# Kernel optimization log

Hardware: AMD Instinct MI355X
Metric: run time of the kernel (lower is better)

The kernel has to match this reference:

```python
import jax, jax.numpy as jnp
import numpy as np

NUM_NODES = 50000
HIDDEN = 128
NUM_REL = 8
NUM_EDGES = 600000


def setup_inputs() -> dict:
    key = jax.random.key(0)
    ks = jax.random.split(key, 10)
    s = 1.0 / np.sqrt(HIDDEN)
    return {
        "edge_index": jax.random.randint(ks[0], (2, NUM_EDGES), 0, NUM_NODES, dtype=jnp.int32),
        "edge_type": jax.random.randint(ks[1], (NUM_EDGES,), 0, NUM_REL, dtype=jnp.int32),
        "node_emb": jax.random.normal(ks[2], (NUM_NODES, HIDDEN), jnp.float32),
        "W1": jax.random.normal(ks[3], (NUM_REL, HIDDEN, HIDDEN), jnp.float32) * s,
        "root1": jax.random.normal(ks[4], (HIDDEN, HIDDEN), jnp.float32) * s,
        "b1": jnp.zeros((HIDDEN,), jnp.float32),
        "W2": jax.random.normal(ks[5], (NUM_REL, HIDDEN, HIDDEN), jnp.float32) * s,
        "root2": jax.random.normal(ks[6], (HIDDEN, HIDDEN), jnp.float32) * s,
        "b2": jnp.zeros((HIDDEN,), jnp.float32),
    }


def rgcn_layer(x, W, root, bias, src, dst, rel):
    # PyG RGCNConv: per-relation MEAN aggregation of neighbor features,
    # transformed by relation weight, plus root transform and bias.
    N = x.shape[0]
    R = W.shape[0]
    # transform node features by every relation weight: [N, R, F]
    xw = jnp.einsum('nd,rdf->nrf', x, W)
    # per-(dst, relation) in-edge counts for mean normalization
    cnt = jnp.zeros((N, R), x.dtype).at[dst, rel].add(1.0)
    inv = 1.0 / jnp.maximum(cnt, 1.0)
    # per-edge message, normalized by destination's per-relation degree
    msg = xw[src, rel] * inv[dst, rel][:, None]  # [E, F]
    agg = jnp.zeros((N, W.shape[2]), x.dtype).at[dst].add(msg)
    return agg + x @ root + bias


def reference(edge_index, edge_type, node_emb, W1, root1, b1, W2, root2, b2):
    src, dst = edge_index[0], edge_index[1]
    h = jax.nn.relu(rgcn_layer(node_emb, W1, root1, b1, src, dst, edge_type))
    out = rgcn_layer(h, W2, root2, b2, src, dst, edge_type)
    return out
```

## Files before the change

kernel.cpp:

```cpp
#include <hip/hip_runtime.h>

#define H 128
#define RREL 8
#define NJ 9

typedef short bf16x8 __attribute__((ext_vector_type(8)));
typedef float f32x4 __attribute__((ext_vector_type(4)));
typedef unsigned short u16x8 __attribute__((ext_vector_type(8)));

static __device__ __forceinline__ unsigned short f2bf(float f) {
    unsigned int u = __float_as_uint(f);
    unsigned int r = (u + 0x7fffu + ((u >> 16) & 1u)) >> 16;
    return (unsigned short)r;
}
static __device__ __forceinline__ float bf2f(unsigned short u) {
    return __uint_as_float(((unsigned int)u) << 16);
}

__global__ void zero_kernel(int* p, long n) {
    long i = (long)blockIdx.x * blockDim.x + threadIdx.x;
    long stride = (long)gridDim.x * blockDim.x;
    for (; i < n; i += stride) p[i] = 0;
}

__global__ void count_kernel(const int* __restrict__ ei, const int* __restrict__ et,
                             int* __restrict__ cnt, int E) {
    int e = blockIdx.x * 256 + threadIdx.x;
    if (e >= E) return;
    int d = ei[E + e];
    int r = et[e];
    atomicAdd(&cnt[(size_t)d * RREL + r], 1);
}

__global__ void scan_block_kernel(const int* __restrict__ cnt, int* __restrict__ rploc,
                                  int* __restrict__ bsum, int N) {
    __shared__ int s[256];
    int t = threadIdx.x;
    int d = blockIdx.x * 256 + t;
    int v = 0;
    if (d < N) {
#pragma unroll
        for (int r = 0; r < RREL; ++r) v += cnt[(size_t)d * RREL + r];
    }
    s[t] = v;
    __syncthreads();
#pragma unroll
    for (int off = 1; off < 256; off <<= 1) {
        int u = 0;
        if (t >= off) u = s[t - off];
        __syncthreads();
        s[t] += u;
        __syncthreads();
    }
    if (d < N) rploc[d] = s[t] - v;
    if (t == 255) bsum[blockIdx.x] = s[255];
}

__global__ void scan_top_kernel(const int* __restrict__ bsum, int* __restrict__ boff, int nb) {
    __shared__ int s[256];
    int t = threadIdx.x;
    int v = (t < nb) ? bsum[t] : 0;
    s[t] = v;
    __syncthreads();
#pragma unroll
    for (int off = 1; off < 256; off <<= 1) {
        int u = 0;
        if (t >= off) u = s[t - off];
        __syncthreads();
        s[t] += u;
        __syncthreads();
    }
    boff[t] = s[t] - v;
}

__global__ void finalize_kernel(const int* __restrict__ cnt, const int* __restrict__ rploc,
                                const int* __restrict__ boff, int* __restrict__ rowptr,
                                float* __restrict__ inv, int N) {
    int d = blockIdx.x * 256 + threadIdx.x;
    if (d >= N) return;
    int rp = rploc[d] + boff[d >> 8];
    rowptr[d] = rp;
    int deg = 0;
#pragma unroll
    for (int r = 0; r < RREL; ++r) {
        int c = cnt[(size_t)d * RREL + r];
        inv[(size_t)d * RREL + r] = 1.0f / (float)max(c, 1);
        deg += c;
    }
    if (d == N - 1) rowptr[N] = rp + deg;
}

__global__ void fill_kernel(const int* __restrict__ ei, const int* __restrict__ et,
                            int* __restrict__ cursor, const int* __restrict__ rowptr,
                            int* __restrict__ packed, int E) {
    int e = blockIdx.x * 256 + threadIdx.x;
    if (e >= E) return;
    int d = ei[E + e];
    int pos = rowptr[d] + atomicAdd(&cursor[d], 1);
    packed[pos] = ei[e] | (et[e] << 20);
}

__global__ void tobf_kernel(const float* __restrict__ x, unsigned short* __restrict__ xb, long n) {
    long i = (long)blockIdx.x * blockDim.x + threadIdx.x;
    long stride = (long)gridDim.x * blockDim.x;
    for (; i < n; i += stride) xb[i] = f2bf(x[i]);
}

__global__ void wcat_kernel(const float* __restrict__ W1, const float* __restrict__ r1,
                            const float* __restrict__ W2, const float* __restrict__ r2,
                            const float* __restrict__ b1, const float* __restrict__ b2,
                            unsigned short* __restrict__ WTa1, unsigned short* __restrict__ WTa2,
                            float* __restrict__ biasP) {
    int id = blockIdx.x * 256 + threadIdx.x;
    const int per = NJ * H * H;
    if (id < per) {
        int j = id / (H * H);
        int fk = id - j * (H * H);
        int f = fk >> 7, k = fk & 127;
        float v = (j < RREL) ? W1[((size_t)j * H + k) * H + f] : r1[(size_t)k * H + f];
        WTa1[id] = f2bf(v);
        int ko = (k & 7) * 16 + (k >> 3);
        float v2 = (j < RREL) ? W2[((size_t)j * H + ko) * H + f] : r2[(size_t)ko * H + f];
        WTa2[id] = f2bf(v2);
    } else if (id < per + 2 * H) {
        int c = id - per;
        int cp = c & 127;
        int co = (cp & 7) * 16 + (cp >> 3);
        biasP[c] = (c < H) ? b1[co] : b2[co];
    }
}

__global__ __launch_bounds__(256) void xw_kernel(const unsigned short* __restrict__ xin,
                                                 const unsigned short* __restrict__ WTa,
                                                 unsigned short* __restrict__ Y,
                                                 int N, int j0, int j1) {
    __shared__ unsigned short Ws[128][136];
    const int t = threadIdx.x;
    const int w = t >> 6, l = t & 63;
    const int m_base = blockIdx.x * 128;
    const int colb = l & 15, quad = l >> 4;
    const f32x4 fz = {0.f, 0.f, 0.f, 0.f};

    int row0 = m_base + w * 32 + colb;
    int row1 = row0 + 16;
    const unsigned short* xr0 = xin + (size_t)(row0 < N ? row0 : N - 1) * H;
    const unsigned short* xr1 = xin + (size_t)(row1 < N ? row1 : N - 1) * H;

    for (int j = j0; j < j1; ++j) {
        __syncthreads();
#pragma unroll
        for (int p = 0; p < 8; ++p) {
            int c = p * 256 + t;
            int f = c >> 4, k8 = (c & 15) * 8;
            *(u16x8*)&Ws[f][k8] = *(const u16x8*)&WTa[((size_t)j * H + f) * H + k8];
        }
        __syncthreads();
        f32x4 acc[2][8];
#pragma unroll
        for (int mi = 0; mi < 2; ++mi)
#pragma unroll
            for (int n = 0; n < 8; ++n) acc[mi][n] = fz;
#pragma unroll
        for (int ks = 0; ks < 4; ++ks) {
            int kl = ks * 32 + quad * 8;
            bf16x8 a0 = *(const bf16x8*)&xr0[kl];
            bf16x8 a1 = *(const bf16x8*)&xr1[kl];
#pragma unroll
            for (int n = 0; n < 8; ++n) {
                bf16x8 b = *(const bf16x8*)&Ws[n * 16 + colb][kl];
                acc[0][n] = __builtin_amdgcn_mfma_f32_16x16x32_bf16(a0, b, acc[0][n], 0, 0, 0);
                acc[1][n] = __builtin_amdgcn_mfma_f32_16x16x32_bf16(a1, b, acc[1][n], 0, 0, 0);
            }
        }
        unsigned short* Yj = Y + (size_t)(j - j0) * N * H;
#pragma unroll
        for (int mi = 0; mi < 2; ++mi) {
#pragma unroll
            for (int i = 0; i < 4; ++i) {
                int row = m_base + w * 32 + mi * 16 + quad * 4 + i;
                if (row < N) {
                    u16x8 o;
#pragma unroll
                    for (int n = 0; n < 8; ++n) o[n] = f2bf(acc[mi][n][i]);
                    *(u16x8*)&Yj[(size_t)row * H + colb * 8] = o;
                }
            }
        }
    }
}

__global__ __launch_bounds__(256) void gather_kernel(const unsigned short* __restrict__ Y,
                                                     const float* __restrict__ inv,
                                                     const int* __restrict__ rowptr,
                                                     const int* __restrict__ packed,
                                                     const float* __restrict__ biasP,
                                                     float* __restrict__ accf,
                                                     float* __restrict__ outf,
                                                     unsigned short* __restrict__ outb,
                                                     int N, int relu, int j0, int j1, int final_pass) {
    const int t = threadIdx.x;
    const int l = t & 63;
    int d = blockIdx.x * 16 + (t >> 4);
    if (d >= N) return;
    const int fl = l & 15;
    const int kc = fl * 8;
    const int gbase = l & 48;
    int rp = 0;
    if (fl < 2) rp = rowptr[d + fl];
    float ivl = 0.f;
    if (fl < 8) ivl = inv[(size_t)d * RREL + fl];
    int beg = __shfl(rp, gbase);
    int end = __shfl(rp, gbase + 1);
    const int jr = (j1 < RREL) ? j1 : RREL;
    float tot[8] = {};
    for (int i = beg; i < end; i += 16) {
        int pk = (i + fl < end) ? packed[i + fl] : 0;
        int m = end - i;
        if (m > 16) m = 16;
        int e = 0;
        for (; e + 1 < m; e += 2) {
            int v0 = __shfl(pk, gbase + e);
            int v1 = __shfl(pk, gbase + e + 1);
            int s0 = v0 & 0xFFFFF, r0 = v0 >> 20;
            int s1 = v1 & 0xFFFFF, r1 = v1 >> 20;
            if (r0 >= j0 && r0 < jr) {
                float iv = __shfl(ivl, gbase + r0);
                u16x8 v = *(const u16x8*)&Y[((size_t)(r0 - j0) * N + s0) * H + kc];
#pragma unroll
                for (int j = 0; j < 8; ++j) tot[j] += iv * bf2f((unsigned short)v[j]);
            }
            if (r1 >= j0 && r1 < jr) {
                float iv = __shfl(ivl, gbase + r1);
                u16x8 v = *(const u16x8*)&Y[((size_t)(r1 - j0) * N + s1) * H + kc];
#pragma unroll
                for (int j = 0; j < 8; ++j) tot[j] += iv * bf2f((unsigned short)v[j]);
            }
        }
        if (e < m) {
            int v0 = __shfl(pk, gbase + e);
            int s0 = v0 & 0xFFFFF, r0 = v0 >> 20;
            if (r0 >= j0 && r0 < jr) {
                float iv = __shfl(ivl, gbase + r0);
                u16x8 v = *(const u16x8*)&Y[((size_t)(r0 - j0) * N + s0) * H + kc];
#pragma unroll
                for (int j = 0; j < 8; ++j) tot[j] += iv * bf2f((unsigned short)v[j]);
            }
        }
    }
    if (j1 == NJ) {
        u16x8 vr = *(const u16x8*)&Y[((size_t)(RREL - j0) * N + d) * H + kc];
#pragma unroll
        for (int j = 0; j < 8; ++j) tot[j] += bf2f((unsigned short)vr[j]);
    }
    if (j0 > 0) {
        f32x4 p0 = *(const f32x4*)&accf[(size_t)d * H + kc];
        f32x4 p1 = *(const f32x4*)&accf[(size_t)d * H + kc + 4];
#pragma unroll
        for (int j = 0; j < 4; ++j) { tot[j] += p0[j]; tot[4 + j] += p1[j]; }
    }
    if (final_pass) {
        f32x4 b0 = *(const f32x4*)&biasP[kc];
        f32x4 b1 = *(const f32x4*)&biasP[kc + 4];
#pragma unroll
        for (int j = 0; j < 4; ++j) { tot[j] += b0[j]; tot[4 + j] += b1[j]; }
        if (relu) {
#pragma unroll
            for (int j = 0; j < 8; ++j) tot[j] = fmaxf(tot[j], 0.f);
        }
        if (outf) {
#pragma unroll
            for (int j = 0; j < 8; ++j) outf[(size_t)d * H + j * 16 + fl] = tot[j];
        } else {
            u16x8 o;
#pragma unroll
            for (int j = 0; j < 8; ++j) o[j] = f2bf(tot[j]);
            *(u16x8*)&outb[(size_t)d * H + kc] = o;
        }
    } else {
        f32x4 o0, o1;
#pragma unroll
        for (int j = 0; j < 4; ++j) { o0[j] = tot[j]; o1[j] = tot[4 + j]; }
        *(f32x4*)&accf[(size_t)d * H + kc] = o0;
        *(f32x4*)&accf[(size_t)d * H + kc + 4] = o1;
    }
}

extern "C" void kernel_launch(void* const* d_in, const int* in_sizes, int n_in,
                              void* d_out, int out_size, void* d_ws, size_t ws_size,
                              hipStream_t stream) {
    const int* edge_index = (const int*)d_in[0];
    const int* edge_type  = (const int*)d_in[1];
    const float* node_emb = (const float*)d_in[2];
    const float* W1    = (const float*)d_in[3];
    const float* root1 = (const float*)d_in[4];
    const float* b1    = (const float*)d_in[5];
    const float* W2    = (const float*)d_in[6];
    const float* root2 = (const float*)d_in[7];
    const float* b2    = (const float*)d_in[8];
    float* out = (float*)d_out;

    const int E = in_sizes[1];
    const int N = in_sizes[2] / H;

    char* base = (char*)d_ws;
    size_t off = 0;
    auto take = [&](size_t bytes) { size_t o = off; off = (off + bytes + 63) & ~(size_t)63; return o; };
    int*   cnt     = (int*)  (base + take((size_t)N * RREL * 4));
    int*   cursor  = (int*)  (base + take((size_t)N * 4));
    int*   rploc   = (int*)  (base + take((size_t)N * 4));
    int*   bsum    = (int*)  (base + take(256 * 4));
    int*   boff    = (int*)  (base + take(256 * 4));
    int*   rowptr  = (int*)  (base + take(((size_t)N + 1) * 4));
    float* inv     = (float*)(base + take((size_t)N * RREL * 4));
    int*   packed  = (int*)  (base + take((size_t)E * 4));
    unsigned short* WTa1 = (unsigned short*)(base + take((size_t)NJ * H * H * 2));
    unsigned short* WTa2 = (unsigned short*)(base + take((size_t)NJ * H * H * 2));
    float* biasP   = (float*)(base + take(2 * H * 4));
    unsigned short* xb  = (unsigned short*)(base + take((size_t)N * H * 2));
    unsigned short* hb  = (unsigned short*)(base + take((size_t)N * H * 2));

    size_t fixed_off = off;
    unsigned short* Y;
    float* accf = nullptr;
    int rc;
    size_t availA = (ws_size > fixed_off) ? ws_size - fixed_off : 0;
    if (availA >= (size_t)NJ * N * H * 2) {
        Y = (unsigned short*)(base + fixed_off);
        rc = NJ;
    } else {
        accf = (float*)(base + fixed_off);
        size_t off2 = fixed_off + (((size_t)N * H * 4 + 63) & ~(size_t)63);
        Y = (unsigned short*)(base + off2);
        size_t availB = (ws_size > off2) ? ws_size - off2 : 0;
        rc = (int)(availB / ((size_t)N * H * 2));
        if (rc > RREL) rc = RREL;
        if (rc < 1) rc = 1;
    }

    const int nbScan = (N + 255) / 256;

    zero_kernel<<<512, 256, 0, stream>>>(cnt, (long)N * (RREL + 1));
    count_kernel<<<(E + 255) / 256, 256, 0, stream>>>(edge_index, edge_type, cnt, E);
    scan_block_kernel<<<nbScan, 256, 0, stream>>>(cnt, rploc, bsum, N);
    scan_top_kernel<<<1, 256, 0, stream>>>(bsum, boff, nbScan);
    finalize_kernel<<<nbScan, 256, 0, stream>>>(cnt, rploc, boff, rowptr, inv, N);
    fill_kernel<<<(E + 255) / 256, 256, 0, stream>>>(edge_index, edge_type, cursor, rowptr, packed, E);
    wcat_kernel<<<(NJ * H * H + 2 * H + 255) / 256, 256, 0, stream>>>(W1, root1, W2, root2, b1, b2,
                                                                      WTa1, WTa2, biasP);
    tobf_kernel<<<1024, 256, 0, stream>>>(node_emb, xb, (long)N * H);

    const int gx = (N + 127) / 128;
    const int gg = (N + 15) / 16;

    auto run_layer = [&](const unsigned short* xin, const unsigned short* WTa, const float* bp,
                         float* of, unsigned short* ob, int relu) {
        for (int j0 = 0; j0 < NJ; j0 += rc) {
            int j1 = (j0 + rc < NJ) ? j0 + rc : NJ;
            int fin = (j1 == NJ);
            xw_kernel<<<gx, 256, 0, stream>>>(xin, WTa, Y, N, j0, j1);
            gather_kernel<<<gg, 256, 0, stream>>>(Y, inv, rowptr, packed, bp, accf,
                                                  fin ? of : nullptr, fin ? ob : nullptr,
                                                  N, relu, j0, j1, fin);
        }
    };

    run_layer(xb, WTa1, biasP, nullptr, hb, 1);
    run_layer(hb, WTa2, biasP + H, out, nullptr, 0);
}
```

Before: 282.1 us.

## Aggregate-then-transform: fuse per-relation gather and GEMM into one layer kernel

Reorders the RGCN computation so raw neighbor features are first summed per (destination, relation) in shared memory, then multiplied by the concatenated relation and root weights with MFMA. This removes the per-relation transformed tensor Y (nine N×H bf16 arrays) and its write and read traffic, and leaves one kernel launch per layer. Edges are now sorted by relation within each destination, using per-(node, relation) row pointers and cursors, so the run-length accumulation works. The cost is a large shared-memory tile per block, which limits occupancy, weights are read from global memory without reuse in LDS, and the per-relation mean is rounded to bf16 before the GEMM.

```diff
diff --git a/kernel.cpp b/kernel.cpp
--- a/kernel.cpp
+++ b/kernel.cpp
@@ -3,6 +3,8 @@
 #define H 128
 #define RREL 8
 #define NJ 9
+#define MT 32
+#define LROW 1160
 
 typedef short bf16x8 __attribute__((ext_vector_type(8)));
 typedef float f32x4 __attribute__((ext_vector_type(4)));
@@ -75,29 +77,32 @@
 
 __global__ void finalize_kernel(const int* __restrict__ cnt, const int* __restrict__ rploc,
                                 const int* __restrict__ boff, int* __restrict__ rowptr,
-                                float* __restrict__ inv, int N) {
+                                int* __restrict__ rowptr2, float* __restrict__ inv, int N) {
     int d = blockIdx.x * 256 + threadIdx.x;
     if (d >= N) return;
     int rp = rploc[d] + boff[d >> 8];
     rowptr[d] = rp;
-    int deg = 0;
+    int run = rp;
 #pragma unroll
     for (int r = 0; r < RREL; ++r) {
         int c = cnt[(size_t)d * RREL + r];
+        rowptr2[(size_t)d * RREL + r] = run;
         inv[(size_t)d * RREL + r] = 1.0f / (float)max(c, 1);
-        deg += c;
-    }
-    if (d == N - 1) rowptr[N] = rp + deg;
+        run += c;
+    }
+    if (d == N - 1) rowptr[N] = run;
 }
 
 __global__ void fill_kernel(const int* __restrict__ ei, const int* __restrict__ et,
-                            int* __restrict__ cursor, const int* __restrict__ rowptr,
+                            int* __restrict__ cursor, const int* __restrict__ rowptr2,
                             int* __restrict__ packed, int E) {
     int e = blockIdx.x * 256 + threadIdx.x;
     if (e >= E) return;
     int d = ei[E + e];
-    int pos = rowptr[d] + atomicAdd(&cursor[d], 1);
-    packed[pos] = ei[e] | (et[e] << 20);
+    int r = et[e];
+    size_t bin = (size_t)d * RREL + r;
+    int pos = rowptr2[bin] + atomicAdd(&cursor[bin], 1);
+    packed[pos] = ei[e] | (r << 20);
 }
 
 __global__ void tobf_kernel(const float* __restrict__ x, unsigned short* __restrict__ xb, long n) {
@@ -117,171 +122,139 @@
         int j = id / (H * H);
         int fk = id - j * (H * H);
         int f = fk >> 7, k = fk & 127;
-        float v = (j < RREL) ? W1[((size_t)j * H + k) * H + f] : r1[(size_t)k * H + f];
-        WTa1[id] = f2bf(v);
-        int ko = (k & 7) * 16 + (k >> 3);
-        float v2 = (j < RREL) ? W2[((size_t)j * H + ko) * H + f] : r2[(size_t)ko * H + f];
+        float v1 = (j < RREL) ? W1[((size_t)j * H + k) * H + f] : r1[(size_t)k * H + f];
+        WTa1[id] = f2bf(v1);
+        float v2 = (j < RREL) ? W2[((size_t)j * H + k) * H + f] : r2[(size_t)k * H + f];
         WTa2[id] = f2bf(v2);
     } else if (id < per + 2 * H) {
         int c = id - per;
-        int cp = c & 127;
-        int co = (cp & 7) * 16 + (cp >> 3);
-        biasP[c] = (c < H) ? b1[co] : b2[co];
-    }
-}
-
-__global__ __launch_bounds__(256) void xw_kernel(const unsigned short* __restrict__ xin,
-                                                 const unsigned short* __restrict__ WTa,
-                                                 unsigned short* __restrict__ Y,
-                                                 int N, int j0, int j1) {
-    __shared__ unsigned short Ws[128][136];
-    const int t = threadIdx.x;
-    const int w = t >> 6, l = t & 63;
-    const int m_base = blockIdx.x * 128;
-    const int colb = l & 15, quad = l >> 4;
-    const f32x4 fz = {0.f, 0.f, 0.f, 0.f};
-
-    int row0 = m_base + w * 32 + colb;
-    int row1 = row0 + 16;
-    const unsigned short* xr0 = xin + (size_t)(row0 < N ? row0 : N - 1) * H;
-    const unsigned short* xr1 = xin + (size_t)(row1 < N ? row1 : N - 1) * H;
-
-    for (int j = j0; j < j1; ++j) {
-        __syncthreads();
-#pragma unroll
-        for (int p = 0; p < 8; ++p) {
-            int c = p * 256 + t;
-            int f = c >> 4, k8 = (c & 15) * 8;
-            *(u16x8*)&Ws[f][k8] = *(const u16x8*)&WTa[((size_t)j * H + f) * H + k8];
-        }
-        __syncthreads();
-        f32x4 acc[2][8];
-#pragma unroll
-        for (int mi = 0; mi < 2; ++mi)
-#pragma unroll
-            for (int n = 0; n < 8; ++n) acc[mi][n] = fz;
-#pragma unroll
-        for (int ks = 0; ks < 4; ++ks) {
-            int kl = ks * 32 + quad * 8;
-            bf16x8 a0 = *(const bf16x8*)&xr0[kl];
-            bf16x8 a1 = *(const bf16x8*)&xr1[kl];
-#pragma unroll
-            for (int n = 0; n < 8; ++n) {
-                bf16x8 b = *(const bf16x8*)&Ws[n * 16 + colb][kl];
-                acc[0][n] = __builtin_amdgcn_mfma_f32_16x16x32_bf16(a0, b, acc[0][n], 0, 0, 0);
-                acc[1][n] = __builtin_amdgcn_mfma_f32_16x16x32_bf16(a1, b, acc[1][n], 0, 0, 0);
-            }
-        }
-        unsigned short* Yj = Y + (size_t)(j - j0) * N * H;
-#pragma unroll
-        for (int mi = 0; mi < 2; ++mi) {
-#pragma unroll
-            for (int i = 0; i < 4; ++i) {
-                int row = m_base + w * 32 + mi * 16 + quad * 4 + i;
-                if (row < N) {
-                    u16x8 o;
-#pragma unroll
-                    for (int n = 0; n < 8; ++n) o[n] = f2bf(acc[mi][n][i]);
-                    *(u16x8*)&Yj[(size_t)row * H + colb * 8] = o;
-                }
-            }
-        }
-    }
-}
-
-__global__ __launch_bounds__(256) void gather_kernel(const unsigned short* __restrict__ Y,
-                                                     const float* __restrict__ inv,
-                                                     const int* __restrict__ rowptr,
-                                                     const int* __restrict__ packed,
-                                                     const float* __restrict__ biasP,
-                                                     float* __restrict__ accf,
-                                                     float* __restrict__ outf,
-                                                     unsigned short* __restrict__ outb,
-                                                     int N, int relu, int j0, int j1, int final_pass) {
+        biasP[c] = (c < H) ? b1[c] : b2[c - H];
+    }
+}
+
+__global__ __launch_bounds__(512) void layer_kernel(const unsigned short* __restrict__ xin,
+                                                    const unsigned short* __restrict__ WTa,
+                                                    const float* __restrict__ biasP,
+                                                    const float* __restrict__ inv,
+                                                    const int* __restrict__ rowptr,
+                                                    const int* __restrict__ packed,
+                                                    float* __restrict__ outf,
+                                                    unsigned short* __restrict__ outb,
+                                                    int N, int relu) {
+    __shared__ __align__(16) unsigned short aggS[MT * LROW];
     const int t = threadIdx.x;
     const int l = t & 63;
-    int d = blockIdx.x * 16 + (t >> 4);
-    if (d >= N) return;
-    const int fl = l & 15;
-    const int kc = fl * 8;
+    const int w = t >> 6;
+    const int g16 = t >> 4;
+    const int fl = t & 15;
     const int gbase = l & 48;
+    const int Mbase = blockIdx.x * MT;
+    const int d = Mbase + g16;
+    const bool valid = d < N;
+
+    unsigned short* rowp = &aggS[g16 * LROW];
+    {
+        u16x8 z = {0, 0, 0, 0, 0, 0, 0, 0};
+#pragma unroll
+        for (int c = 0; c < 8; ++c) *(u16x8*)&rowp[(c * 16 + fl) * 8] = z;
+        if (valid) {
+            *(u16x8*)&rowp[RREL * H + fl * 8] = *(const u16x8*)&xin[(size_t)d * H + fl * 8];
+        } else {
+            *(u16x8*)&rowp[RREL * H + fl * 8] = z;
+        }
+    }
+
     int rp = 0;
-    if (fl < 2) rp = rowptr[d + fl];
+    if (valid && fl < 2) rp = rowptr[d + fl];
     float ivl = 0.f;
-    if (fl < 8) ivl = inv[(size_t)d * RREL + fl];
+    if (valid && fl < 8) ivl = inv[(size_t)d * RREL + fl];
     int beg = __shfl(rp, gbase);
     int end = __shfl(rp, gbase + 1);
-    const int jr = (j1 < RREL) ? j1 : RREL;
-    float tot[8] = {};
+
+    float tmp[8] = {};
+    float ivc = 0.f;
+    int rcur = -1;
     for (int i = beg; i < end; i += 16) {
         int pk = (i + fl < end) ? packed[i + fl] : 0;
         int m = end - i;
         if (m > 16) m = 16;
-        int e = 0;
-        for (; e + 1 < m; e += 2) {
-            int v0 = __shfl(pk, gbase + e);
-            int v1 = __shfl(pk, gbase + e + 1);
-            int s0 = v0 & 0xFFFFF, r0 = v0 >> 20;
-            int s1 = v1 & 0xFFFFF, r1 = v1 >> 20;
-            if (r0 >= j0 && r0 < jr) {
-                float iv = __shfl(ivl, gbase + r0);
-                u16x8 v = *(const u16x8*)&Y[((size_t)(r0 - j0) * N + s0) * H + kc];
-#pragma unroll
-                for (int j = 0; j < 8; ++j) tot[j] += iv * bf2f((unsigned short)v[j]);
+        for (int e = 0; e < m; ++e) {
+            int v = __shfl(pk, gbase + e);
+            int s = v & 0xFFFFF, r = v >> 20;
+            if (r != rcur) {
+                if (rcur >= 0) {
+                    u16x8 o;
+#pragma unroll
+                    for (int j = 0; j < 8; ++j) o[j] = f2bf(ivc * tmp[j]);
+                    *(u16x8*)&rowp[rcur * H + fl * 8] = o;
+                }
+                rcur = r;
+                ivc = __shfl(ivl, gbase + r);
+#pragma unroll
+                for (int j = 0; j < 8; ++j) tmp[j] = 0.f;
             }
-            if (r1 >= j0 && r1 < jr) {
-                float iv = __shfl(ivl, gbase + r1);
-                u16x8 v = *(const u16x8*)&Y[((size_t)(r1 - j0) * N + s1) * H + kc];
-#pragma unroll
-                for (int j = 0; j < 8; ++j) tot[j] += iv * bf2f((unsigned short)v[j]);
+            u16x8 xv = *(const u16x8*)&xin[(size_t)s * H + fl * 8];
+#pragma unroll
+            for (int j = 0; j < 8; ++j) tmp[j] += bf2f((unsigned short)xv[j]);
+        }
+    }
+    if (rcur >= 0) {
+        u16x8 o;
+#pragma unroll
+        for (int j = 0; j < 8; ++j) o[j] = f2bf(ivc * tmp[j]);
+        *(u16x8*)&rowp[rcur * H + fl * 8] = o;
+    }
+
+    __syncthreads();
+
+    const int colb = l & 15, quad = l >> 4;
+    const int fcol = w * 16 + colb;
+    const f32x4 fz = {0.f, 0.f, 0.f, 0.f};
+    f32x4 acc0 = fz, acc1 = fz;
+    const unsigned short* arow0 = &aggS[colb * LROW];
+    const unsigned short* arow1 = &aggS[(16 + colb) * LROW];
+#pragma unroll
+    for (int j = 0; j < NJ; ++j) {
+#pragma unroll
+        for (int ks = 0; ks < 4; ++ks) {
+            const int kl = ks * 32 + quad * 8;
+            bf16x8 b = *(const bf16x8*)&WTa[((size_t)j * H + fcol) * H + kl];
+            bf16x8 a0 = *(const bf16x8*)&arow0[j * H + kl];
+            bf16x8 a1 = *(const bf16x8*)&arow1[j * H + kl];
+            acc0 = __builtin_amdgcn_mfma_f32_16x16x32_bf16(a0, b, acc0, 0, 0, 0);
+            acc1 = __builtin_amdgcn_mfma_f32_16x16x32_bf16(a1, b, acc1, 0, 0, 0);
+        }
+    }
+
+    __syncthreads();
+    float* stg = (float*)aggS;
+    const float bcol = biasP[fcol];
+#pragma unroll
+    for (int i = 0; i < 4; ++i) {
+        float v0 = acc0[i] + bcol;
+        float v1 = acc1[i] + bcol;
+        if (relu) { v0 = fmaxf(v0, 0.f); v1 = fmaxf(v1, 0.f); }
+        stg[(quad * 4 + i) * 132 + fcol] = v0;
+        stg[(16 + quad * 4 + i) * 132 + fcol] = v1;
+    }
+    __syncthreads();
+    {
+        int row = t >> 4;
+        int dd = Mbase + row;
+        if (dd < N) {
+            int c0 = fl * 8;
+            f32x4 p0 = *(const f32x4*)&stg[row * 132 + c0];
+            f32x4 p1 = *(const f32x4*)&stg[row * 132 + c0 + 4];
+            if (outf) {
+                *(f32x4*)&outf[(size_t)dd * H + c0] = p0;
+                *(f32x4*)&outf[(size_t)dd * H + c0 + 4] = p1;
+            } else {
+                u16x8 o;
+#pragma unroll
+                for (int j = 0; j < 4; ++j) { o[j] = f2bf(p0[j]); o[4 + j] = f2bf(p1[j]); }
+                *(u16x8*)&outb[(size_t)dd * H + c0] = o;
             }
         }
-        if (e < m) {
-            int v0 = __shfl(pk, gbase + e);
-            int s0 = v0 & 0xFFFFF, r0 = v0 >> 20;
-            if (r0 >= j0 && r0 < jr) {
-                float iv = __shfl(ivl, gbase + r0);
-                u16x8 v = *(const u16x8*)&Y[((size_t)(r0 - j0) * N + s0) * H + kc];
-#pragma unroll
-                for (int j = 0; j < 8; ++j) tot[j] += iv * bf2f((unsigned short)v[j]);
-            }
-        }
-    }
-    if (j1 == NJ) {
-        u16x8 vr = *(const u16x8*)&Y[((size_t)(RREL - j0) * N + d) * H + kc];
-#pragma unroll
-        for (int j = 0; j < 8; ++j) tot[j] += bf2f((unsigned short)vr[j]);
-    }
-    if (j0 > 0) {
-        f32x4 p0 = *(const f32x4*)&accf[(size_t)d * H + kc];
-        f32x4 p1 = *(const f32x4*)&accf[(size_t)d * H + kc + 4];
-#pragma unroll
-        for (int j = 0; j < 4; ++j) { tot[j] += p0[j]; tot[4 + j] += p1[j]; }
-    }
-    if (final_pass) {
-        f32x4 b0 = *(const f32x4*)&biasP[kc];
-        f32x4 b1 = *(const f32x4*)&biasP[kc + 4];
-#pragma unroll
-        for (int j = 0; j < 4; ++j) { tot[j] += b0[j]; tot[4 + j] += b1[j]; }
-        if (relu) {
-#pragma unroll
-            for (int j = 0; j < 8; ++j) tot[j] = fmaxf(tot[j], 0.f);
-        }
-        if (outf) {
-#pragma unroll
-            for (int j = 0; j < 8; ++j) outf[(size_t)d * H + j * 16 + fl] = tot[j];
-        } else {
-            u16x8 o;
-#pragma unroll
-            for (int j = 0; j < 8; ++j) o[j] = f2bf(tot[j]);
-            *(u16x8*)&outb[(size_t)d * H + kc] = o;
-        }
-    } else {
-        f32x4 o0, o1;
-#pragma unroll
-        for (int j = 0; j < 4; ++j) { o0[j] = tot[j]; o1[j] = tot[4 + j]; }
-        *(f32x4*)&accf[(size_t)d * H + kc] = o0;
-        *(f32x4*)&accf[(size_t)d * H + kc + 4] = o1;
     }
 }
 
@@ -306,11 +279,12 @@
     size_t off = 0;
     auto take = [&](size_t bytes) { size_t o = off; off = (off + bytes + 63) & ~(size_t)63; return o; };
     int*   cnt     = (int*)  (base + take((size_t)N * RREL * 4));
-    int*   cursor  = (int*)  (base + take((size_t)N * 4));
+    int*   cursor8 = (int*)  (base + take((size_t)N * RREL * 4));
     int*   rploc   = (int*)  (base + take((size_t)N * 4));
     int*   bsum    = (int*)  (base + take(256 * 4));
     int*   boff    = (int*)  (base + take(256 * 4));
     int*   rowptr  = (int*)  (base + take(((size_t)N + 1) * 4));
+    int*   rowptr2 = (int*)  (base + take((size_t)N * RREL * 4));
     float* inv     = (float*)(base + take((size_t)N * RREL * 4));
     int*   packed  = (int*)  (base + take((size_t)E * 4));
     unsigned short* WTa1 = (unsigned short*)(base + take((size_t)NJ * H * H * 2));
@@ -318,52 +292,23 @@
     float* biasP   = (float*)(base + take(2 * H * 4));
     unsigned short* xb  = (unsigned short*)(base + take((size_t)N * H * 2));
     unsigned short* hb  = (unsigned short*)(base + take((size_t)N * H * 2));
-
-    size_t fixed_off = off;
-    unsigned short* Y;
-    float* accf = nullptr;
-    int rc;
-    size_t availA = (ws_size > fixed_off) ? ws_size - fixed_off : 0;
-    if (availA >= (size_t)NJ * N * H * 2) {
-        Y = (unsigned short*)(base + fixed_off);
-        rc = NJ;
-    } else {
-        accf = (float*)(base + fixed_off);
-        size_t off2 = fixed_off + (((size_t)N * H * 4 + 63) & ~(size_t)63);
-        Y = (unsigned short*)(base + off2);
-        size_t availB = (ws_size > off2) ? ws_size - off2 : 0;
-        rc = (int)(availB / ((size_t)N * H * 2));
-        if (rc > RREL) rc = RREL;
-        if (rc < 1) rc = 1;
-    }
+    (void)ws_size;
 
     const int nbScan = (N + 255) / 256;
 
-    zero_kernel<<<512, 256, 0, stream>>>(cnt, (long)N * (RREL + 1));
+    zero_kernel<<<512, 256, 0, stream>>>(cnt, (long)N * (2 * RREL));
     count_kernel<<<(E + 255) / 256, 256, 0, stream>>>(edge_index, edge_type, cnt, E);
     scan_block_kernel<<<nbScan, 256, 0, stream>>>(cnt, rploc, bsum, N);
     scan_top_kernel<<<1, 256, 0, stream>>>(bsum, boff, nbScan);
-    finalize_kernel<<<nbScan, 256, 0, stream>>>(cnt, rploc, boff, rowptr, inv, N);
-    fill_kernel<<<(E + 255) / 256, 256, 0, stream>>>(edge_index, edge_type, cursor, rowptr, packed, E);
+    finalize_kernel<<<nbScan, 256, 0, stream>>>(cnt, rploc, boff, rowptr, rowptr2, inv, N);
+    fill_kernel<<<(E + 255) / 256, 256, 0, stream>>>(edge_index, edge_type, cursor8, rowptr2, packed, E);
     wcat_kernel<<<(NJ * H * H + 2 * H + 255) / 256, 256, 0, stream>>>(W1, root1, W2, root2, b1, b2,
                                                                       WTa1, WTa2, biasP);
     tobf_kernel<<<1024, 256, 0, stream>>>(node_emb, xb, (long)N * H);
 
-    const int gx = (N + 127) / 128;
-    const int gg = (N + 15) / 16;
-
-    auto run_layer = [&](const unsigned short* xin, const unsigned short* WTa, const float* bp,
-                         float* of, unsigned short* ob, int relu) {
-        for (int j0 = 0; j0 < NJ; j0 += rc) {
-            int j1 = (j0 + rc < NJ) ? j0 + rc : NJ;
-            int fin = (j1 == NJ);
-            xw_kernel<<<gx, 256, 0, stream>>>(xin, WTa, Y, N, j0, j1);
-            gather_kernel<<<gg, 256, 0, stream>>>(Y, inv, rowptr, packed, bp, accf,
-                                                  fin ? of : nullptr, fin ? ob : nullptr,
-                                                  N, relu, j0, j1, fin);
-        }
-    };
-
-    run_layer(xb, WTa1, biasP, nullptr, hb, 1);
-    run_layer(hb, WTa2, biasP + H, out, nullptr, 0);
-}
+    const int gl = (N + MT - 1) / MT;
+    layer_kernel<<<gl, 512, 0, stream>>>(xb, WTa1, biasP, inv, rowptr, packed,
+                                         nullptr, hb, N, 1);
+    layer_kernel<<<gl, 512, 0, stream>>>(hb, WTa2, biasP + H, inv, rowptr, packed,
+                                         out, nullptr, N, 0);
+}
```

Measured after the change: 366.0 us. 29.7% more time.
